# Kernel tuning notes

Measured on AMD Instinct MI355X. Metric: run time of the kernel, lower is better.

Reference implementation:

```python
import jax, jax.numpy as jnp
import numpy as np

B, T, D, H = 4, 2048, 1024, 16
HD = D // H  # head_dim = 64


def setup_inputs() -> dict:
    key = jax.random.key(0)
    k1, k2, k3 = jax.random.split(key, 3)
    x = jax.random.normal(k1, (B, T, D), dtype=jnp.float32)
    # rotary cache: (T, head_dim/2, 2) holding (cos, sin)
    inv_freq = 1.0 / (10000.0 ** (jnp.arange(0, HD, 2, dtype=jnp.float32) / HD))  # (HD/2,)
    t = jnp.arange(T, dtype=jnp.float32)
    freqs = jnp.einsum('t,f->tf', t, inv_freq)  # (T, HD/2)
    rope = jnp.stack([jnp.cos(freqs), jnp.sin(freqs)], axis=-1)  # (T, HD/2, 2)
    # causal boolean attn mask, broadcastable (1,1,T,T)
    mask = jnp.tril(jnp.ones((T, T), dtype=bool))[None, None]
    # params (bias-free linears), scaled like nn.Linear default init
    W_attn = jax.random.normal(k2, (3 * D, D), dtype=jnp.float32) / np.sqrt(D)
    W_proj = jax.random.normal(k3, (D, D), dtype=jnp.float32) / np.sqrt(D)
    return {"x": x, "rope": rope, "mask": mask, "W_attn": W_attn, "W_proj": W_proj}


def apply_rope(x, rope):
    # x: (B, T, H, HD); rope: (T, HD/2, 2)
    b, t, h, hd = x.shape
    xr = x.reshape(b, t, h, hd // 2, 2)
    x1, x2 = xr[..., 0], xr[..., 1]
    cos = rope[None, :, None, :, 0]  # (1, T, 1, HD/2)
    sin = rope[None, :, None, :, 1]
    out = jnp.stack([x1 * cos - x2 * sin, x1 * sin + x2 * cos], axis=-1)
    return out.reshape(b, t, h, hd)


def reference(x, rope, mask, W_attn, W_proj):
    b, t, d = x.shape
    qkv = jnp.einsum('btd,ed->bte', x, W_attn)  # (B, T, 3D)
    q, k, v = jnp.split(qkv, 3, axis=2)
    q = apply_rope(q.reshape(b, t, H, HD), rope)
    k = apply_rope(k.reshape(b, t, H, HD), rope)
    v = v.reshape(b, t, H, HD)
    # (B, H, T, HD)
    q = q.transpose(0, 2, 1, 3)
    k = k.transpose(0, 2, 1, 3)
    v = v.transpose(0, 2, 1, 3)
    scale = 1.0 / np.sqrt(HD)
    scores = jnp.einsum('bhqd,bhkd->bhqk', q, k) * scale
    scores = jnp.where(mask, scores, jnp.finfo(scores.dtype).min)
    attn = jax.nn.softmax(scores, axis=-1)
    o = jnp.einsum('bhqk,bhkd->bhqd', attn, v)
    o = o.transpose(0, 2, 1, 3).reshape(b, t, d)
    return jnp.einsum('btd,ed->bte', o, W_proj)
```

## Files before the change

kernel.cpp:

```cpp
#include <hip/hip_runtime.h>

typedef unsigned short u16;
typedef unsigned int u32;
typedef unsigned long long u64;
typedef __bf16 v8bf __attribute__((ext_vector_type(8)));
typedef __bf16 v4bf __attribute__((ext_vector_type(4)));
typedef float v4f __attribute__((ext_vector_type(4)));
typedef float v16f __attribute__((ext_vector_type(16)));

#define BB 4
#define TT 2048
#define HH 16
#define DD 1024

__device__ __forceinline__ u16 f2bf(float f){
  u32 u = __float_as_uint(f);
  u32 r = u + 0x7FFFu + ((u >> 16) & 1u);
  return (u16)(r >> 16);
}
__device__ __forceinline__ float bf2f(u16 h){ return __uint_as_float(((u32)h) << 16); }
__device__ __forceinline__ v16f z16(){
  v16f z;
#pragma unroll
  for (int i = 0; i < 16; i++) z[i] = 0.f;
  return z;
}

typedef __attribute__((address_space(1))) const void gas_t;
typedef __attribute__((address_space(3))) void las_t;
__device__ __forceinline__ void gl_lds16(const void* g, void* l){
  __builtin_amdgcn_global_load_lds((gas_t*)g, (las_t*)l, 16, 0, 0);
}

__global__ __launch_bounds__(256) void k_convert(
    const float* __restrict__ x, const float* __restrict__ wa,
    const float* __restrict__ wp, u16* __restrict__ xb,
    u16* __restrict__ wab, u16* __restrict__ wpb){
  int i = blockIdx.x * 256 + threadIdx.x;
  const int nxq = (BB*TT*DD) / 4;
  const int naq = (3*DD*DD) / 4;
  const float* src; u16* dst; int j;
  if (i < nxq)            { src = x;  dst = xb;  j = i; }
  else if (i < nxq + naq) { src = wa; dst = wab; j = i - nxq; }
  else                    { src = wp; dst = wpb; j = i - nxq - naq; }
  float4 v = reinterpret_cast<const float4*>(src)[j];
  u64 p = (u64)f2bf(v.x) | ((u64)f2bf(v.y) << 16)
        | ((u64)f2bf(v.z) << 32) | ((u64)f2bf(v.w) << 48);
  reinterpret_cast<u64*>(dst)[j] = p;
}

__global__ __launch_bounds__(256) void k_gemm_bt(
    const u16* __restrict__ A, const u16* __restrict__ Bt,
    int M, int N, int K, int mode, float* __restrict__ Cf,
    u16* __restrict__ qo, u16* __restrict__ ko, u16* __restrict__ vo){
  __shared__ char smem[32768];
  char* As = smem;
  char* Bs = smem + 16384;
  const int t = threadIdx.x;
  const int lane = t & 63, w = t >> 6;
  const int c = lane & 15, g = lane >> 4;
  const int nbn = N >> 7;
  const int bm = blockIdx.x / nbn, bn = blockIdx.x % nbn;
  const long arow0 = (long)bm * 128;
  const long brow0 = (long)bn * 128;
  const int wrow = (w >> 1) * 64, wcol = (w & 1) * 64;

  v4f acc[4][4];
#pragma unroll
  for (int i = 0; i < 4; i++)
#pragma unroll
    for (int j = 0; j < 4; j++){ v4f z = {0.f,0.f,0.f,0.f}; acc[i][j] = z; }

  for (int k0 = 0; k0 < K; k0 += 64){
    __syncthreads();
#pragma unroll
    for (int i = 0; i < 4; i++){
      int slot = t + i * 256;
      int row  = slot >> 3;
      int cb   = (slot & 7) << 4;
      int scb  = cb ^ ((row & 7) << 4);
      gl_lds16((const char*)A  + ((arow0 + row) * (long)K + k0) * 2 + scb,
               As + ((t & 192) + i * 256) * 16);
      gl_lds16((const char*)Bt + ((brow0 + row) * (long)K + k0) * 2 + scb,
               Bs + ((t & 192) + i * 256) * 16);
    }
    __syncthreads();

    v8bf af[4][2], bfr[4][2];
#pragma unroll
    for (int mt = 0; mt < 4; mt++){
      int row = wrow + mt * 16 + c;
      int sw  = (row & 7) << 4;
#pragma unroll
      for (int ks = 0; ks < 2; ks++)
        af[mt][ks] = *(const v8bf*)(As + row * 128 + ((ks * 64 + g * 16) ^ sw));
    }
#pragma unroll
    for (int nt = 0; nt < 4; nt++){
      int row = wcol + nt * 16 + c;
      int sw  = (row & 7) << 4;
#pragma unroll
      for (int ks = 0; ks < 2; ks++)
        bfr[nt][ks] = *(const v8bf*)(Bs + row * 128 + ((ks * 64 + g * 16) ^ sw));
    }
#pragma unroll
    for (int mt = 0; mt < 4; mt++)
#pragma unroll
      for (int nt = 0; nt < 4; nt++)
#pragma unroll
        for (int ks = 0; ks < 2; ks++)
          acc[mt][nt] = __builtin_amdgcn_mfma_f32_16x16x32_bf16(
              af[mt][ks], bfr[nt][ks], acc[mt][nt], 0, 0, 0);
  }

  if (mode == 1){
#pragma unroll
    for (int mt = 0; mt < 4; mt++)
#pragma unroll
      for (int nt = 0; nt < 4; nt++)
#pragma unroll
        for (int r = 0; r < 4; r++){
          long row = arow0 + wrow + mt * 16 + g * 4 + r;
          long col = brow0 + wcol + nt * 16 + c;
          Cf[row * N + col] = acc[mt][nt][r];
        }
  } else {
    long bb = arow0 >> 11;
#pragma unroll
    for (int mt = 0; mt < 4; mt++)
#pragma unroll
      for (int nt = 0; nt < 4; nt++){
        int e    = (int)brow0 + wcol + nt * 16 + c;
        int tsel = e >> 10;
        int h    = (e >> 6) & 15;
        int d    = e & 63;
        long tpos = (arow0 & 2047) + wrow + mt * 16 + g * 4;
        if (tsel == 2){
          v4bf pk;
#pragma unroll
          for (int r = 0; r < 4; r++) pk[r] = (__bf16)acc[mt][nt][r];
          *(v4bf*)(vo + (((bb * HH + h) * 64 + d) << 11) + tpos) = pk;
        } else {
          u16* dst = tsel ? ko : qo;
#pragma unroll
          for (int r = 0; r < 4; r++)
            dst[((bb * HH + h) * TT + tpos + r) * 64 + d] = f2bf(acc[mt][nt][r]);
        }
      }
  }
}

__global__ __launch_bounds__(256) void k_rope2(
    u16* __restrict__ qb, u16* __restrict__ kb, const float* __restrict__ rope){
  int tid   = blockIdx.x * 256 + threadIdx.x;
  int which = tid >> 20;
  int r     = tid & 1048575;
  int s     = r & 7;
  int row   = r >> 3;
  int tpos  = row & 2047;
  u16* base = (which ? kb : qb) + (long)row * 64 + s * 8;
  int4 w0 = *(const int4*)base;
  float4 r01 = *(const float4*)(rope + tpos * 64 + s * 8);
  float4 r23 = *(const float4*)(rope + tpos * 64 + s * 8 + 4);
  float cs[4] = {r01.x, r01.z, r23.x, r23.z};
  float sn[4] = {r01.y, r01.w, r23.y, r23.w};
  float scale = which ? 1.0f : 0.18033688011112042f;
  int wv[4] = {w0.x, w0.y, w0.z, w0.w};
  int ov[4];
#pragma unroll
  for (int j = 0; j < 4; j++){
    float x1 = bf2f((u16)((u32)wv[j] & 0xffffu));
    float x2 = bf2f((u16)((u32)wv[j] >> 16));
    float oe = (x1 * cs[j] - x2 * sn[j]) * scale;
    float od = (x1 * sn[j] + x2 * cs[j]) * scale;
    ov[j] = (int)((u32)f2bf(oe) | ((u32)f2bf(od) << 16));
  }
  int4 out = {ov[0], ov[1], ov[2], ov[3]};
  *(int4*)base = out;
}

__global__ __launch_bounds__(256) void k_attn(
    const u16* __restrict__ Q, const u16* __restrict__ K,
    const u16* __restrict__ Vt, u16* __restrict__ O){
  __shared__ char smem[32768];
  char* ksm = smem;
  char* vsm = smem + 8192;
  char* psm = smem + 16384;
  int bx = blockIdx.x;
  int bt = 15 - (bx >> 6);
  int bh = bx & 63;
  int q0 = bt * 128;
  int b = bh >> 4, h = bh & 15;
  const u16* Qb = Q  + (size_t)bh * TT * 64;
  const u16* Kb = K  + (size_t)bh * TT * 64;
  const u16* Vb = Vt + (size_t)bh * 64 * TT;
  const int t = threadIdx.x, lane = t & 63, w = t >> 6;
  const int c = lane & 31, hi = lane >> 5;
  const int wq0 = q0 + w * 32;
  const int swz = (c & 7) << 4;
  char* prow = psm + (w * 32 + c) * 128;

  v8bf qf[4];
  {
    const u16* qrow = Qb + (size_t)(wq0 + c) * 64 + hi * 8;
#pragma unroll
    for (int kc = 0; kc < 4; kc++) qf[kc] = *(const v8bf*)(qrow + kc * 16);
  }

  float m_ = -1e30f, l_ = 0.f;
  v16f accO0 = z16(), accO1 = z16();

  for (int kv0 = 0; kv0 < q0 + 128; kv0 += 64){
    __syncthreads();
#pragma unroll
    for (int i = 0; i < 2; i++){
      int s   = t + i * 256;
      int row = s >> 3;
      int cb  = (s & 7) << 4;
      int scb = cb ^ ((row & 7) << 4);
      gl_lds16((const char*)Kb + (size_t)(kv0 + row) * 128 + scb,
               ksm + ((t & 192) + i * 256) * 16);
      gl_lds16((const char*)Vb + (size_t)row * (TT * 2) + (size_t)kv0 * 2 + scb,
               vsm + ((t & 192) + i * 256) * 16);
    }
    __syncthreads();

    if (kv0 <= wq0 + 31){
      v16f s0 = z16(), s1 = z16();
#pragma unroll
      for (int kc = 0; kc < 4; kc++){
        int off = (kc * 32 + hi * 16) ^ swz;
        v8bf a0 = *(const v8bf*)(ksm + c * 128 + off);
        v8bf a1 = *(const v8bf*)(ksm + (32 + c) * 128 + off);
        s0 = __builtin_amdgcn_mfma_f32_32x32x16_bf16(a0, qf[kc], s0, 0, 0, 0);
        s1 = __builtin_amdgcn_mfma_f32_32x32x16_bf16(a1, qf[kc], s1, 0, 0, 0);
      }
      if (kv0 + 63 > wq0){
        int q = wq0 + c;
#pragma unroll
        for (int r = 0; r < 16; r++){
          int crow = (r & 3) + 8 * (r >> 2) + 4 * hi;
          if (kv0 + crow > q)      s0[r] = -1e30f;
          if (kv0 + 32 + crow > q) s1[r] = -1e30f;
        }
      }
      float mx = -1e30f;
#pragma unroll
      for (int r = 0; r < 16; r++){ mx = fmaxf(mx, s0[r]); mx = fmaxf(mx, s1[r]); }
      mx = fmaxf(mx, __shfl_xor(mx, 32, 64));
      float mn = fmaxf(m_, mx);
      float alpha = __builtin_amdgcn_exp2f(m_ - mn);
      m_ = mn;
      float sum = 0.f;
#pragma unroll
      for (int r = 0; r < 16; r++){
        float p0 = __builtin_amdgcn_exp2f(s0[r] - mn);
        float p1 = __builtin_amdgcn_exp2f(s1[r] - mn);
        s0[r] = p0; s1[r] = p1;
        sum += p0 + p1;
      }
      sum += __shfl_xor(sum, 32, 64);
      l_ = l_ * alpha + sum;
#pragma unroll
      for (int q4 = 0; q4 < 4; q4++){
        v4bf pk0, pk1;
#pragma unroll
        for (int j = 0; j < 4; j++){
          pk0[j] = (__bf16)s0[q4 * 4 + j];
          pk1[j] = (__bf16)s1[q4 * 4 + j];
        }
        *(v4bf*)(prow + ((q4 * 16 + hi * 8) ^ swz))      = pk0;
        *(v4bf*)(prow + ((64 + q4 * 16 + hi * 8) ^ swz)) = pk1;
      }
#pragma unroll
      for (int r = 0; r < 16; r++){ accO0[r] *= alpha; accO1[r] *= alpha; }
      v8bf pb[4];
#pragma unroll
      for (int kc = 0; kc < 4; kc++)
        pb[kc] = *(const v8bf*)(prow + ((kc * 32 + hi * 16) ^ swz));
#pragma unroll
      for (int kc = 0; kc < 4; kc++){
        int off = (kc * 32 + hi * 16) ^ swz;
        v8bf va0 = *(const v8bf*)(vsm + c * 128 + off);
        v8bf va1 = *(const v8bf*)(vsm + (32 + c) * 128 + off);
        accO0 = __builtin_amdgcn_mfma_f32_32x32x16_bf16(va0, pb[kc], accO0, 0, 0, 0);
        accO1 = __builtin_amdgcn_mfma_f32_32x32x16_bf16(va1, pb[kc], accO1, 0, 0, 0);
      }
    }
  }

  float inv = __builtin_amdgcn_rcpf(l_);
  int q = wq0 + c;
  u16* orow = O + ((size_t)(b * TT + q)) * DD + h * 64;
#pragma unroll
  for (int q4 = 0; q4 < 4; q4++){
    v4bf o0, o1;
#pragma unroll
    for (int j = 0; j < 4; j++){
      o0[j] = (__bf16)(accO0[q4 * 4 + j] * inv);
      o1[j] = (__bf16)(accO1[q4 * 4 + j] * inv);
    }
    *(v4bf*)(orow + q4 * 8 + hi * 4)      = o0;
    *(v4bf*)(orow + 32 + q4 * 8 + hi * 4) = o1;
  }
}

extern "C" void kernel_launch(void* const* d_in, const int* in_sizes, int n_in,
                              void* d_out, int out_size, void* d_ws, size_t ws_size,
                              hipStream_t stream){
  const float* x    = (const float*)d_in[0];
  const float* rope = (const float*)d_in[1];
  const float* Wa   = (const float*)d_in[3];
  const float* Wp   = (const float*)d_in[4];

  char* ws = (char*)d_ws;
  u16* xb  = (u16*)(ws);
  u16* wab = (u16*)(ws + (16u << 20));
  u16* wpb = (u16*)(ws + (22u << 20));
  u16* qb  = (u16*)(ws + (24u << 20));
  u16* kb  = (u16*)(ws + (40u << 20));
  u16* vtb = (u16*)(ws + (56u << 20));
  u16* ob  = xb;

  k_convert<<<dim3(12288), dim3(256), 0, stream>>>(x, Wa, Wp, xb, wab, wpb);
  k_gemm_bt<<<dim3(24 * 64), dim3(256), 0, stream>>>(
      xb, wab, 8192, 3072, 1024, 0, nullptr, qb, kb, vtb);
  k_rope2<<<dim3(8192), dim3(256), 0, stream>>>(qb, kb, rope);
  k_attn<<<dim3(1024), dim3(256), 0, stream>>>(qb, kb, vtb, ob);
  k_gemm_bt<<<dim3(8 * 64), dim3(256), 0, stream>>>(
      ob, wpb, 8192, 1024, 1024, 1, (float*)d_out, nullptr, nullptr, nullptr);
}
```

Measured before the change: 184.2 us.

## Pair causal q-tiles per block, keep P in registers, skip unneeded rescale

Each attention block now handles two query tiles, a long one (15-pr) and a short one (pr), so every block does equal causal work. The launch drops to 512 blocks. The P matrix is no longer staged through shared memory. It is packed with v_cvt_pk_bf16_f32 and rearranged across lanes with v_permlane32_swap so it can feed the PV MFMA directly, which cuts LDS to 16KB and removes the write/read round trip. The online-softmax rescale of the accumulators is skipped when no lane's max grew; this adds a wave-wide vote and branch in exchange.

```diff
diff --git a/kernel.cpp b/kernel.cpp
--- a/kernel.cpp
+++ b/kernel.cpp
@@ -7,6 +7,7 @@
 typedef __bf16 v4bf __attribute__((ext_vector_type(4)));
 typedef float v4f __attribute__((ext_vector_type(4)));
 typedef float v16f __attribute__((ext_vector_type(16)));
+typedef u32 v4u __attribute__((ext_vector_type(4)));
 
 #define BB 4
 #define TT 2048
@@ -24,6 +25,14 @@
 #pragma unroll
   for (int i = 0; i < 16; i++) z[i] = 0.f;
   return z;
+}
+__device__ __forceinline__ u32 cvtpk(float lo, float hi){
+  u32 d;
+  asm("v_cvt_pk_bf16_f32 %0, %1, %2" : "=v"(d) : "v"(lo), "v"(hi));
+  return d;
+}
+__device__ __forceinline__ void swap32(u32 &a, u32 &b){
+  asm volatile("v_permlane32_swap_b32 %0, %1" : "+v"(a), "+v"(b));
 }
 
 typedef __attribute__((address_space(1))) const void gas_t;
@@ -182,126 +191,136 @@
 __global__ __launch_bounds__(256) void k_attn(
     const u16* __restrict__ Q, const u16* __restrict__ K,
     const u16* __restrict__ Vt, u16* __restrict__ O){
-  __shared__ char smem[32768];
+  __shared__ char smem[16384];
   char* ksm = smem;
   char* vsm = smem + 8192;
-  char* psm = smem + 16384;
   int bx = blockIdx.x;
-  int bt = 15 - (bx >> 6);
   int bh = bx & 63;
-  int q0 = bt * 128;
+  int pr = bx >> 6;
   int b = bh >> 4, h = bh & 15;
   const u16* Qb = Q  + (size_t)bh * TT * 64;
   const u16* Kb = K  + (size_t)bh * TT * 64;
   const u16* Vb = Vt + (size_t)bh * 64 * TT;
   const int t = threadIdx.x, lane = t & 63, w = t >> 6;
   const int c = lane & 31, hi = lane >> 5;
-  const int wq0 = q0 + w * 32;
   const int swz = (c & 7) << 4;
-  char* prow = psm + (w * 32 + c) * 128;
-
-  v8bf qf[4];
-  {
-    const u16* qrow = Qb + (size_t)(wq0 + c) * 64 + hi * 8;
-#pragma unroll
-    for (int kc = 0; kc < 4; kc++) qf[kc] = *(const v8bf*)(qrow + kc * 16);
-  }
-
-  float m_ = -1e30f, l_ = 0.f;
-  v16f accO0 = z16(), accO1 = z16();
-
-  for (int kv0 = 0; kv0 < q0 + 128; kv0 += 64){
-    __syncthreads();
-#pragma unroll
-    for (int i = 0; i < 2; i++){
-      int s   = t + i * 256;
-      int row = s >> 3;
-      int cb  = (s & 7) << 4;
-      int scb = cb ^ ((row & 7) << 4);
-      gl_lds16((const char*)Kb + (size_t)(kv0 + row) * 128 + scb,
-               ksm + ((t & 192) + i * 256) * 16);
-      gl_lds16((const char*)Vb + (size_t)row * (TT * 2) + (size_t)kv0 * 2 + scb,
-               vsm + ((t & 192) + i * 256) * 16);
-    }
-    __syncthreads();
-
-    if (kv0 <= wq0 + 31){
-      v16f s0 = z16(), s1 = z16();
-#pragma unroll
-      for (int kc = 0; kc < 4; kc++){
-        int off = (kc * 32 + hi * 16) ^ swz;
-        v8bf a0 = *(const v8bf*)(ksm + c * 128 + off);
-        v8bf a1 = *(const v8bf*)(ksm + (32 + c) * 128 + off);
-        s0 = __builtin_amdgcn_mfma_f32_32x32x16_bf16(a0, qf[kc], s0, 0, 0, 0);
-        s1 = __builtin_amdgcn_mfma_f32_32x32x16_bf16(a1, qf[kc], s1, 0, 0, 0);
+
+  for (int pass = 0; pass < 2; pass++){
+    int bt = pass ? pr : (15 - pr);
+    int q0 = bt * 128;
+    int wq0 = q0 + w * 32;
+
+    v8bf qf[4];
+    {
+      const u16* qrow = Qb + (size_t)(wq0 + c) * 64 + hi * 8;
+#pragma unroll
+      for (int kc = 0; kc < 4; kc++) qf[kc] = *(const v8bf*)(qrow + kc * 16);
+    }
+
+    float m_ = -1e30f, l_ = 0.f;
+    v16f accO0 = z16(), accO1 = z16();
+
+    for (int kv0 = 0; kv0 < q0 + 128; kv0 += 64){
+      __syncthreads();
+#pragma unroll
+      for (int i = 0; i < 2; i++){
+        int s   = t + i * 256;
+        int row = s >> 3;
+        int cb  = (s & 7) << 4;
+        int scb = cb ^ ((row & 7) << 4);
+        gl_lds16((const char*)Kb + (size_t)(kv0 + row) * 128 + scb,
+                 ksm + ((t & 192) + i * 256) * 16);
+        gl_lds16((const char*)Vb + (size_t)row * (TT * 2) + (size_t)kv0 * 2 + scb,
+                 vsm + ((t & 192) + i * 256) * 16);
       }
-      if (kv0 + 63 > wq0){
-        int q = wq0 + c;
+      __syncthreads();
+
+      if (kv0 <= wq0 + 31){
+        v16f s0 = z16(), s1 = z16();
+#pragma unroll
+        for (int kc = 0; kc < 4; kc++){
+          int off = (kc * 32 + hi * 16) ^ swz;
+          v8bf a0 = *(const v8bf*)(ksm + c * 128 + off);
+          v8bf a1 = *(const v8bf*)(ksm + (32 + c) * 128 + off);
+          s0 = __builtin_amdgcn_mfma_f32_32x32x16_bf16(a0, qf[kc], s0, 0, 0, 0);
+          s1 = __builtin_amdgcn_mfma_f32_32x32x16_bf16(a1, qf[kc], s1, 0, 0, 0);
+        }
+        if (kv0 + 63 > wq0){
+          int q = wq0 + c;
+#pragma unroll
+          for (int r = 0; r < 16; r++){
+            int crow = (r & 3) + 8 * (r >> 2) + 4 * hi;
+            if (kv0 + crow > q)      s0[r] = -1e30f;
+            if (kv0 + 32 + crow > q) s1[r] = -1e30f;
+          }
+        }
+        float mx = -1e30f;
+#pragma unroll
+        for (int r = 0; r < 16; r++){ mx = fmaxf(mx, s0[r]); mx = fmaxf(mx, s1[r]); }
+        mx = fmaxf(mx, __shfl_xor(mx, 32, 64));
+        if (!__all(mx <= m_)){
+          float mn = fmaxf(m_, mx);
+          float alpha = __builtin_amdgcn_exp2f(m_ - mn);
+          m_ = mn;
+          l_ *= alpha;
+#pragma unroll
+          for (int r = 0; r < 16; r++){ accO0[r] *= alpha; accO1[r] *= alpha; }
+        }
+        float sum = 0.f;
 #pragma unroll
         for (int r = 0; r < 16; r++){
-          int crow = (r & 3) + 8 * (r >> 2) + 4 * hi;
-          if (kv0 + crow > q)      s0[r] = -1e30f;
-          if (kv0 + 32 + crow > q) s1[r] = -1e30f;
+          float p0 = __builtin_amdgcn_exp2f(s0[r] - m_);
+          float p1 = __builtin_amdgcn_exp2f(s1[r] - m_);
+          s0[r] = p0; s1[r] = p1;
+          sum += p0 + p1;
+        }
+        sum += __shfl_xor(sum, 32, 64);
+        l_ += sum;
+        v8bf pbf[4];
+        {
+          u32 wd[16];
+#pragma unroll
+          for (int i = 0; i < 8; i++) wd[i]     = cvtpk(s0[2*i], s0[2*i+1]);
+#pragma unroll
+          for (int i = 0; i < 8; i++) wd[8 + i] = cvtpk(s1[2*i], s1[2*i+1]);
+          swap32(wd[0], wd[2]);  swap32(wd[1], wd[3]);
+          swap32(wd[4], wd[6]);  swap32(wd[5], wd[7]);
+          swap32(wd[8], wd[10]); swap32(wd[9], wd[11]);
+          swap32(wd[12], wd[14]); swap32(wd[13], wd[15]);
+          v4u u0 = {wd[0], wd[1], wd[2], wd[3]};
+          v4u u1 = {wd[4], wd[5], wd[6], wd[7]};
+          v4u u2 = {wd[8], wd[9], wd[10], wd[11]};
+          v4u u3 = {wd[12], wd[13], wd[14], wd[15]};
+          pbf[0] = __builtin_bit_cast(v8bf, u0);
+          pbf[1] = __builtin_bit_cast(v8bf, u1);
+          pbf[2] = __builtin_bit_cast(v8bf, u2);
+          pbf[3] = __builtin_bit_cast(v8bf, u3);
+        }
+#pragma unroll
+        for (int kc = 0; kc < 4; kc++){
+          int off = (kc * 32 + hi * 16) ^ swz;
+          v8bf va0 = *(const v8bf*)(vsm + c * 128 + off);
+          v8bf va1 = *(const v8bf*)(vsm + (32 + c) * 128 + off);
+          accO0 = __builtin_amdgcn_mfma_f32_32x32x16_bf16(va0, pbf[kc], accO0, 0, 0, 0);
+          accO1 = __builtin_amdgcn_mfma_f32_32x32x16_bf16(va1, pbf[kc], accO1, 0, 0, 0);
         }
       }
-      float mx = -1e30f;
-#pragma unroll
-      for (int r = 0; r < 16; r++){ mx = fmaxf(mx, s0[r]); mx = fmaxf(mx, s1[r]); }
-      mx = fmaxf(mx, __shfl_xor(mx, 32, 64));
-      float mn = fmaxf(m_, mx);
-      float alpha = __builtin_amdgcn_exp2f(m_ - mn);
-      m_ = mn;
-      float sum = 0.f;
-#pragma unroll
-      for (int r = 0; r < 16; r++){
-        float p0 = __builtin_amdgcn_exp2f(s0[r] - mn);
-        float p1 = __builtin_amdgcn_exp2f(s1[r] - mn);
-        s0[r] = p0; s1[r] = p1;
-        sum += p0 + p1;
+    }
+
+    float inv = __builtin_amdgcn_rcpf(l_);
+    int q = wq0 + c;
+    u16* orow = O + ((size_t)(b * TT + q)) * DD + h * 64;
+#pragma unroll
+    for (int q4 = 0; q4 < 4; q4++){
+      v4bf o0, o1;
+#pragma unroll
+      for (int j = 0; j < 4; j++){
+        o0[j] = (__bf16)(accO0[q4 * 4 + j] * inv);
+        o1[j] = (__bf16)(accO1[q4 * 4 + j] * inv);
       }
-      sum += __shfl_xor(sum, 32, 64);
-      l_ = l_ * alpha + sum;
-#pragma unroll
-      for (int q4 = 0; q4 < 4; q4++){
-        v4bf pk0, pk1;
-#pragma unroll
-        for (int j = 0; j < 4; j++){
-          pk0[j] = (__bf16)s0[q4 * 4 + j];
-          pk1[j] = (__bf16)s1[q4 * 4 + j];
-        }
-        *(v4bf*)(prow + ((q4 * 16 + hi * 8) ^ swz))      = pk0;
-        *(v4bf*)(prow + ((64 + q4 * 16 + hi * 8) ^ swz)) = pk1;
-      }
-#pragma unroll
-      for (int r = 0; r < 16; r++){ accO0[r] *= alpha; accO1[r] *= alpha; }
-      v8bf pb[4];
-#pragma unroll
-      for (int kc = 0; kc < 4; kc++)
-        pb[kc] = *(const v8bf*)(prow + ((kc * 32 + hi * 16) ^ swz));
-#pragma unroll
-      for (int kc = 0; kc < 4; kc++){
-        int off = (kc * 32 + hi * 16) ^ swz;
-        v8bf va0 = *(const v8bf*)(vsm + c * 128 + off);
-        v8bf va1 = *(const v8bf*)(vsm + (32 + c) * 128 + off);
-        accO0 = __builtin_amdgcn_mfma_f32_32x32x16_bf16(va0, pb[kc], accO0, 0, 0, 0);
-        accO1 = __builtin_amdgcn_mfma_f32_32x32x16_bf16(va1, pb[kc], accO1, 0, 0, 0);
-      }
-    }
-  }
-
-  float inv = __builtin_amdgcn_rcpf(l_);
-  int q = wq0 + c;
-  u16* orow = O + ((size_t)(b * TT + q)) * DD + h * 64;
-#pragma unroll
-  for (int q4 = 0; q4 < 4; q4++){
-    v4bf o0, o1;
-#pragma unroll
-    for (int j = 0; j < 4; j++){
-      o0[j] = (__bf16)(accO0[q4 * 4 + j] * inv);
-      o1[j] = (__bf16)(accO1[q4 * 4 + j] * inv);
-    }
-    *(v4bf*)(orow + q4 * 8 + hi * 4)      = o0;
-    *(v4bf*)(orow + 32 + q4 * 8 + hi * 4) = o1;
+      *(v4bf*)(orow + q4 * 8 + hi * 4)      = o0;
+      *(v4bf*)(orow + 32 + q4 * 8 + hi * 4) = o1;
+    }
   }
 }
 
@@ -326,7 +345,7 @@
   k_gemm_bt<<<dim3(24 * 64), dim3(256), 0, stream>>>(
       xb, wab, 8192, 3072, 1024, 0, nullptr, qb, kb, vtb);
   k_rope2<<<dim3(8192), dim3(256), 0, stream>>>(qb, kb, rope);
-  k_attn<<<dim3(1024), dim3(256), 0, stream>>>(qb, kb, vtb, ob);
+  k_attn<<<dim3(512), dim3(256), 0, stream>>>(qb, kb, vtb, ob);
   k_gemm_bt<<<dim3(8 * 64), dim3(256), 0, stream>>>(
       ob, wpb, 8192, 1024, 1024, 1, (float*)d_out, nullptr, nullptr, nullptr);
 }
```

After: 181.4 us. Within noise of the previous version (-1.5%).
